# Performance work log

Measured on AMD Instinct MI355X. Metric: run time of the kernel, lower is better.

The kernel has to match this reference:

```python
import jax, jax.numpy as jnp
import numpy as np

B, S, D, E, K = 4, 2048, 1024, 8, 2
H = 4 * D  # FFN hidden per expert


def setup_inputs() -> dict:
    key = jax.random.key(0)
    ks = jax.random.split(key, 5)
    s = 0.02  # init scale
    return {
        "x": jax.random.normal(ks[0], (B, S, D), dtype=jnp.float32),
        "Wg": jax.random.normal(ks[1], (D, E), dtype=jnp.float32) * s,
        "bg": jnp.zeros((E,), dtype=jnp.float32),
        "W1": jax.random.normal(ks[2], (E, D, H), dtype=jnp.float32) * s,
        "b1": jnp.zeros((E, H), dtype=jnp.float32),
        "W2": jax.random.normal(ks[3], (E, H, D), dtype=jnp.float32) * s,
        "b2": jnp.zeros((E, D), dtype=jnp.float32),
    }


def reference(x, Wg, bg, W1, b1, W2, b2):
    # Router: softmax over expert logits, then top-k (torch.topk semantics)
    probs = jax.nn.softmax(x @ Wg + bg, axis=-1)      # [B,S,E]
    w, idx = jax.lax.top_k(probs, K)                   # [B,S,K] each
    # Dense all-experts MLP (matches original: every expert runs on every token)
    h = jax.nn.gelu(jnp.einsum('bsd,edh->bseh', x, W1) + b1, approximate=False)  # [B,S,E,H]
    y = jnp.einsum('bseh,ehd->bsed', h, W2) + b2       # [B,S,E,D]
    # One-hot mask + weighted sum == gather selected experts, scale by w, sum over k
    yk = jnp.take_along_axis(y, idx[..., None], axis=2)  # [B,S,K,D]
    return jnp.sum(yk * w[..., None], axis=2)            # [B,S,D]
```

## Files before the change

### kernel.cpp

```cpp
#include <hip/hip_runtime.h>
#include <hip/hip_bf16.h>
#include <math.h>


#define TOK     8192
#define DMODEL  1024
#define NEXP    8
#define HFF     4096
#define NASSIGN 16384
#define SLOTPAD 16512
#define BM      128
#define BN      128
#define BK      64
#define MAXRT   135

typedef __attribute__((ext_vector_type(8))) short s16x8;
typedef __attribute__((ext_vector_type(4))) float f32x4;

__device__ __forceinline__ void gll16(const void* g, void* l) {
  __builtin_amdgcn_global_load_lds((const __attribute__((address_space(1))) void*)g,
                                   (__attribute__((address_space(3))) void*)l, 16, 0, 0);
}

__global__ void transpose_cvt(const float* __restrict__ in, __hip_bfloat16* __restrict__ out,
                              int R, int C) {
  __shared__ float t[64][65];
  const float* src = in + (size_t)blockIdx.z * R * C;
  __hip_bfloat16* dst = out + (size_t)blockIdx.z * R * C;
  const int r0 = blockIdx.y * 64, c0 = blockIdx.x * 64;
  const int tc = threadIdx.x & 63, tr = threadIdx.x >> 6;
#pragma unroll
  for (int i = 0; i < 16; ++i) {
    int r = i * 4 + tr;
    t[r][tc] = src[(size_t)(r0 + r) * C + c0 + tc];
  }
  __syncthreads();
  const int jl = (threadIdx.x & 15) * 4;
  const int cw = threadIdx.x >> 4;
#pragma unroll
  for (int p = 0; p < 4; ++p) {
    const int cc = p * 16 + cw;
    union { ushort4 u; __hip_bfloat16 h[4]; } o;
#pragma unroll
    for (int u = 0; u < 4; ++u) o.h[u] = __float2bfloat16(t[jl + u][cc]);
    *(ushort4*)(dst + (size_t)(c0 + cc) * R + r0 + jl) = o.u;
  }
}

__global__ void router_kernel(const float* __restrict__ x, const float* __restrict__ Wg,
                              const float* __restrict__ bg, int* __restrict__ idx,
                              float* __restrict__ wtok, int* __restrict__ counts) {
  __shared__ int scnt[NEXP];
  if (threadIdx.x < NEXP) scnt[threadIdx.x] = 0;
  __syncthreads();
  const int wave = threadIdx.x >> 6, lane = threadIdx.x & 63;
  const int t = blockIdx.x * 4 + wave;
  float acc[NEXP];
#pragma unroll
  for (int e = 0; e < NEXP; ++e) acc[e] = 0.f;
  const float* xr = x + (size_t)t * DMODEL + lane * 16;
#pragma unroll
  for (int j = 0; j < 4; ++j) {
    float4 xv = *(const float4*)(xr + j * 4);
    const float* wr = Wg + (size_t)(lane * 16 + j * 4) * NEXP;
#pragma unroll
    for (int u = 0; u < 4; ++u) {
      float xs = (&xv.x)[u];
      float4 w0 = *(const float4*)(wr + u * NEXP);
      float4 w1 = *(const float4*)(wr + u * NEXP + 4);
      acc[0] += xs * w0.x; acc[1] += xs * w0.y; acc[2] += xs * w0.z; acc[3] += xs * w0.w;
      acc[4] += xs * w1.x; acc[5] += xs * w1.y; acc[6] += xs * w1.z; acc[7] += xs * w1.w;
    }
  }
#pragma unroll
  for (int off = 32; off >= 1; off >>= 1) {
#pragma unroll
    for (int e = 0; e < NEXP; ++e) acc[e] += __shfl_xor(acc[e], off, 64);
  }
  if (lane == 0) {
    float l[NEXP], m = -1e30f;
#pragma unroll
    for (int e = 0; e < NEXP; ++e) { l[e] = acc[e] + bg[e]; m = fmaxf(m, l[e]); }
    float p[NEXP], s = 0.f;
#pragma unroll
    for (int e = 0; e < NEXP; ++e) { p[e] = expf(l[e] - m); s += p[e]; }
    float inv = 1.f / s;
#pragma unroll
    for (int e = 0; e < NEXP; ++e) p[e] *= inv;
    int i0 = 0; float v0 = p[0];
#pragma unroll
    for (int e = 1; e < NEXP; ++e) if (p[e] > v0) { v0 = p[e]; i0 = e; }
    int i1 = -1; float v1 = -1e30f;
#pragma unroll
    for (int e = 0; e < NEXP; ++e) if (e != i0 && p[e] > v1) { v1 = p[e]; i1 = e; }
    idx[2 * t] = i0; idx[2 * t + 1] = i1;
    wtok[2 * t] = v0; wtok[2 * t + 1] = v1;
    atomicAdd(&scnt[i0], 1); atomicAdd(&scnt[i1], 1);
  }
  __syncthreads();
  if (threadIdx.x < NEXP) atomicAdd(&counts[threadIdx.x], scnt[threadIdx.x]);
}

__global__ void scan_kernel(int* ctrl) {
  if (threadIdx.x == 0 && blockIdx.x == 0) {
    int* counts = ctrl;
    int* cursor = ctrl + 8;
    int* expOff = ctrl + 16;
    int* tro = ctrl + 26;
    expOff[0] = 0; tro[0] = 0;
    for (int e = 0; e < NEXP; ++e) {
      expOff[e + 1] = expOff[e] + counts[e];
      tro[e + 1] = tro[e] + (counts[e] + BM - 1) / BM;
      cursor[e] = expOff[e];
    }
  }
}

__global__ void scatter_kernel(const int* __restrict__ idx, const float* __restrict__ wtok,
                               int* ctrl, int* __restrict__ perm, float* __restrict__ wslot) {
  __shared__ int lcnt[NEXP];
  __shared__ int lbase[NEXP];
  const int t = blockIdx.x * 256 + threadIdx.x;
  if (threadIdx.x < NEXP) lcnt[threadIdx.x] = 0;
  __syncthreads();
  const int e0 = idx[2 * t], e1 = idx[2 * t + 1];
  const int l0 = atomicAdd(&lcnt[e0], 1);
  const int l1 = atomicAdd(&lcnt[e1], 1);
  __syncthreads();
  if (threadIdx.x < NEXP)
    lbase[threadIdx.x] = atomicAdd(&ctrl[8 + threadIdx.x], lcnt[threadIdx.x]);
  __syncthreads();
  const int s0 = lbase[e0] + l0, s1 = lbase[e1] + l1;
  perm[s0] = t; perm[s1] = t;
  wslot[s0] = wtok[2 * t]; wslot[s1] = wtok[2 * t + 1];
}

__global__ void gather_cvt_x(const float* __restrict__ x, const int* __restrict__ perm,
                             __hip_bfloat16* __restrict__ xg) {
  const int slot = blockIdx.x;
  const int t = perm[slot];
  const float4 v = *(const float4*)(x + (size_t)t * DMODEL + threadIdx.x * 4);
  union { ushort4 u; __hip_bfloat16 h[4]; } o;
  o.h[0] = __float2bfloat16(v.x); o.h[1] = __float2bfloat16(v.y);
  o.h[2] = __float2bfloat16(v.z); o.h[3] = __float2bfloat16(v.w);
  *(ushort4*)(xg + (size_t)slot * DMODEL + threadIdx.x * 4) = o.u;
}


__global__ __launch_bounds__(256, 3) void gemm1_kernel(
    const __hip_bfloat16* __restrict__ xg, const __hip_bfloat16* __restrict__ w1t,
    const float* __restrict__ b1, __hip_bfloat16* __restrict__ hbuf,
    const int* __restrict__ ctrl) {
  const int* expOff = ctrl + 16;
  const int* tro = ctrl + 26;
  const int w = blockIdx.x;
  const int rt = w >> 5, nt = w & 31;
  if (rt >= tro[NEXP]) return;
  int e = 0;
#pragma unroll
  for (int q = 1; q < NEXP; ++q) if (tro[q] <= rt) e = q;
  const int rowBase = expOff[e] + (rt - tro[e]) * BM;
  const int rowEnd = expOff[e + 1];

  __shared__ __hip_bfloat16 lA[BM * BK];
  __shared__ __hip_bfloat16 lB[BN * BK];

  const int tid = threadIdx.x;
  const int lane = tid & 63, wave = tid >> 6;
  const int quad = lane >> 4, lm = lane & 15;
  const int waveM = (wave >> 1) * 64, waveN = (wave & 1) * 64;

  f32x4 acc[4][4];
#pragma unroll
  for (int a = 0; a < 4; ++a)
#pragma unroll
    for (int b = 0; b < 4; ++b) acc[a][b] = (f32x4){0.f, 0.f, 0.f, 0.f};

  const __hip_bfloat16* bbase = w1t + (size_t)e * HFF * DMODEL + (size_t)nt * BN * DMODEL;
  const __hip_bfloat16* gA[4]; const __hip_bfloat16* gB[4];
  __hip_bfloat16* sA[4]; __hip_bfloat16* sB[4];
#pragma unroll
  for (int i = 0; i < 4; ++i) {
    const int s = tid + 256 * i;
    const int r = s >> 3, sl = s & 7, kc = sl ^ (r & 7);
    gA[i] = xg + (size_t)(rowBase + r) * DMODEL + kc * 8;
    gB[i] = bbase + (size_t)r * DMODEL + kc * 8;
    sA[i] = lA + s * 8; sB[i] = lB + s * 8;
  }

  int aOff[4], bOff[4];
#pragma unroll
  for (int tm = 0; tm < 4; ++tm) {
    int r = waveM + tm * 16 + lm;
    aOff[tm] = r * 64 + (quad ^ (r & 7)) * 8;
  }
#pragma unroll
  for (int tn = 0; tn < 4; ++tn) {
    int r = waveN + tn * 16 + lm;
    bOff[tn] = r * 64 + (quad ^ (r & 7)) * 8;
  }

  for (int kt = 0; kt < DMODEL / BK; ++kt) {
#pragma unroll
    for (int i = 0; i < 4; ++i) { gll16(gA[i], sA[i]); gll16(gB[i], sB[i]); }
#pragma unroll
    for (int i = 0; i < 4; ++i) { gA[i] += BK; gB[i] += BK; }
    __syncthreads();
#pragma unroll
    for (int h = 0; h < 2; ++h) {
      s16x8 af[4], bfr[4];
#pragma unroll
      for (int tm = 0; tm < 4; ++tm) af[tm] = *(const s16x8*)(lA + (aOff[tm] ^ (h * 32)));
#pragma unroll
      for (int tn = 0; tn < 4; ++tn) bfr[tn] = *(const s16x8*)(lB + (bOff[tn] ^ (h * 32)));
#pragma unroll
      for (int tm = 0; tm < 4; ++tm)
#pragma unroll
        for (int tn = 0; tn < 4; ++tn)
          acc[tm][tn] = __builtin_amdgcn_mfma_f32_16x16x32_bf16(af[tm], bfr[tn], acc[tm][tn], 0, 0, 0);
    }
    __syncthreads();
  }

  const int colBase = nt * BN + waveN;
  float bv[4];
#pragma unroll
  for (int tn = 0; tn < 4; ++tn) bv[tn] = b1[e * HFF + colBase + tn * 16 + lm];
#pragma unroll
  for (int tm = 0; tm < 4; ++tm) {
    const int rb = rowBase + waveM + tm * 16 + quad * 4;
#pragma unroll
    for (int reg = 0; reg < 4; ++reg) {
      const int row = rb + reg;
      if (row < rowEnd) {
#pragma unroll
        for (int tn = 0; tn < 4; ++tn) {
          float v = acc[tm][tn][reg] + bv[tn];
          v = 0.5f * v * (1.f + erff(v * 0.70710678118654752f));
          hbuf[(size_t)row * HFF + colBase + tn * 16 + lm] = __float2bfloat16(v);
        }
      }
    }
  }
}

__global__ __launch_bounds__(256, 3) void gemm2_kernel(
    const __hip_bfloat16* __restrict__ hbuf, const __hip_bfloat16* __restrict__ w2t,
    const float* __restrict__ b2, const float* __restrict__ wslot,
    const int* __restrict__ perm, float* __restrict__ out, const int* __restrict__ ctrl) {
  const int* expOff = ctrl + 16;
  const int* tro = ctrl + 26;
  const int w = blockIdx.x;
  const int rt = w >> 3, nt = w & 7;
  if (rt >= tro[NEXP]) return;
  int e = 0;
#pragma unroll
  for (int q = 1; q < NEXP; ++q) if (tro[q] <= rt) e = q;
  const int rowBase = expOff[e] + (rt - tro[e]) * BM;
  const int rowEnd = expOff[e + 1];

  __shared__ __hip_bfloat16 lA[BM * BK];
  __shared__ __hip_bfloat16 lB[BN * BK];

  const int tid = threadIdx.x;
  const int lane = tid & 63, wave = tid >> 6;
  const int quad = lane >> 4, lm = lane & 15;
  const int waveM = (wave >> 1) * 64, waveN = (wave & 1) * 64;

  f32x4 acc[4][4];
#pragma unroll
  for (int a = 0; a < 4; ++a)
#pragma unroll
    for (int b = 0; b < 4; ++b) acc[a][b] = (f32x4){0.f, 0.f, 0.f, 0.f};

  const __hip_bfloat16* bbase = w2t + (size_t)e * DMODEL * HFF + (size_t)nt * BN * HFF;
  const __hip_bfloat16* gA[4]; const __hip_bfloat16* gB[4];
  __hip_bfloat16* sA[4]; __hip_bfloat16* sB[4];
#pragma unroll
  for (int i = 0; i < 4; ++i) {
    const int s = tid + 256 * i;
    const int r = s >> 3, sl = s & 7, kc = sl ^ (r & 7);
    gA[i] = hbuf + (size_t)(rowBase + r) * HFF + kc * 8;
    gB[i] = bbase + (size_t)r * HFF + kc * 8;
    sA[i] = lA + s * 8; sB[i] = lB + s * 8;
  }

  int aOff[4], bOff[4];
#pragma unroll
  for (int tm = 0; tm < 4; ++tm) {
    int r = waveM + tm * 16 + lm;
    aOff[tm] = r * 64 + (quad ^ (r & 7)) * 8;
  }
#pragma unroll
  for (int tn = 0; tn < 4; ++tn) {
    int r = waveN + tn * 16 + lm;
    bOff[tn] = r * 64 + (quad ^ (r & 7)) * 8;
  }

  for (int kt = 0; kt < HFF / BK; ++kt) {
#pragma unroll
    for (int i = 0; i < 4; ++i) { gll16(gA[i], sA[i]); gll16(gB[i], sB[i]); }
#pragma unroll
    for (int i = 0; i < 4; ++i) { gA[i] += BK; gB[i] += BK; }
    __syncthreads();
#pragma unroll
    for (int h = 0; h < 2; ++h) {
      s16x8 af[4], bfr[4];
#pragma unroll
      for (int tm = 0; tm < 4; ++tm) af[tm] = *(const s16x8*)(lA + (aOff[tm] ^ (h * 32)));
#pragma unroll
      for (int tn = 0; tn < 4; ++tn) bfr[tn] = *(const s16x8*)(lB + (bOff[tn] ^ (h * 32)));
#pragma unroll
      for (int tm = 0; tm < 4; ++tm)
#pragma unroll
        for (int tn = 0; tn < 4; ++tn)
          acc[tm][tn] = __builtin_amdgcn_mfma_f32_16x16x32_bf16(af[tm], bfr[tn], acc[tm][tn], 0, 0, 0);
    }
    __syncthreads();
  }

  const int colBase = nt * BN + waveN;
  float bv[4];
#pragma unroll
  for (int tn = 0; tn < 4; ++tn) bv[tn] = b2[e * DMODEL + colBase + tn * 16 + lm];
#pragma unroll
  for (int tm = 0; tm < 4; ++tm) {
    const int rb = rowBase + waveM + tm * 16 + quad * 4;
#pragma unroll
    for (int reg = 0; reg < 4; ++reg) {
      const int row = rb + reg;
      if (row < rowEnd) {
        const float wr = wslot[row];
        float* orow = out + (size_t)perm[row] * DMODEL + colBase;
#pragma unroll
        for (int tn = 0; tn < 4; ++tn)
          atomicAdd(orow + tn * 16 + lm, (acc[tm][tn][reg] + bv[tn]) * wr);
      }
    }
  }
}

extern "C" void kernel_launch(void* const* d_in, const int* in_sizes, int n_in,
                              void* d_out, int out_size, void* d_ws, size_t ws_size,
                              hipStream_t stream) {
  const float* x  = (const float*)d_in[0];
  const float* Wg = (const float*)d_in[1];
  const float* bg = (const float*)d_in[2];
  const float* W1 = (const float*)d_in[3];
  const float* b1 = (const float*)d_in[4];
  const float* W2 = (const float*)d_in[5];
  const float* b2 = (const float*)d_in[6];
  float* out = (float*)d_out;

  char* ws = (char*)d_ws;
  size_t off = 0;
  auto take = [&](size_t bytes) -> char* {
    char* p = ws + off;
    off = (off + bytes + 255) & ~(size_t)255;
    return p;
  };
  int*   ctrl  = (int*)take(64 * sizeof(int));
  int*   idx   = (int*)take((size_t)TOK * 2 * 4);
  float* wtok  = (float*)take((size_t)TOK * 2 * 4);
  int*   perm  = (int*)take((size_t)SLOTPAD * 4);
  float* wslot = (float*)take((size_t)SLOTPAD * 4);
  __hip_bfloat16* W1t = (__hip_bfloat16*)take((size_t)NEXP * HFF * DMODEL * 2);
  __hip_bfloat16* W2t = (__hip_bfloat16*)take((size_t)NEXP * DMODEL * HFF * 2);
  __hip_bfloat16* xgb = (__hip_bfloat16*)take((size_t)SLOTPAD * DMODEL * 2);
  __hip_bfloat16* hb  = (__hip_bfloat16*)take((size_t)SLOTPAD * HFF * 2);
  (void)ws_size; (void)in_sizes; (void)n_in; (void)out_size;

  hipMemsetAsync(ctrl, 0, 64 * sizeof(int), stream);
  hipMemsetAsync(out, 0, (size_t)TOK * DMODEL * 4, stream);
  transpose_cvt<<<dim3(HFF / 64, DMODEL / 64, NEXP), 256, 0, stream>>>(W1, W1t, DMODEL, HFF);
  transpose_cvt<<<dim3(DMODEL / 64, HFF / 64, NEXP), 256, 0, stream>>>(W2, W2t, HFF, DMODEL);
  router_kernel<<<TOK / 4, 256, 0, stream>>>(x, Wg, bg, idx, wtok, ctrl);
  scan_kernel<<<1, 64, 0, stream>>>(ctrl);
  scatter_kernel<<<TOK / 256, 256, 0, stream>>>(idx, wtok, ctrl, perm, wslot);
  gather_cvt_x<<<NASSIGN, 256, 0, stream>>>(x, perm, xgb);
  gemm1_kernel<<<MAXRT * (HFF / BN), 256, 0, stream>>>(xgb, W1t, b1, hb, ctrl);
  gemm2_kernel<<<MAXRT * (DMODEL / BN), 256, 0, stream>>>(hb, W2t, b2, wslot, perm, out, ctrl);
}
```

Baseline: 793.5 us.

## Use 256x256 tiles with double-buffered LDS pipeline and split-K in gemm2

```diff
diff --git a/kernel.cpp b/kernel.cpp
--- a/kernel.cpp
+++ b/kernel.cpp
@@ -8,11 +8,11 @@
 #define NEXP    8
 #define HFF     4096
 #define NASSIGN 16384
-#define SLOTPAD 16512
-#define BM      128
-#define BN      128
+#define SLOTPAD 16640
+#define BM      256
+#define BN      256
 #define BK      64
-#define MAXRT   135
+#define MAXRT   71
 
 typedef __attribute__((ext_vector_type(8))) short s16x8;
 typedef __attribute__((ext_vector_type(4))) float f32x4;
@@ -21,6 +21,18 @@
   __builtin_amdgcn_global_load_lds((const __attribute__((address_space(1))) void*)g,
                                    (__attribute__((address_space(3))) void*)l, 16, 0, 0);
 }
+
+#define MFMA_Q(AFR, BFR, ACC)                                                   \
+  do {                                                                          \
+    __builtin_amdgcn_s_setprio(1);                                              \
+    _Pragma("unroll") for (int tm_ = 0; tm_ < 4; ++tm_) {                       \
+      _Pragma("unroll") for (int tn_ = 0; tn_ < 4; ++tn_) {                     \
+        (ACC)[tm_][tn_] = __builtin_amdgcn_mfma_f32_16x16x32_bf16(              \
+            (AFR)[tm_], (BFR)[tn_], (ACC)[tm_][tn_], 0, 0, 0);                  \
+      }                                                                         \
+    }                                                                           \
+    __builtin_amdgcn_s_setprio(0);                                              \
+  } while (0)
 
 __global__ void transpose_cvt(const float* __restrict__ in, __hip_bfloat16* __restrict__ out,
                               int R, int C) {
@@ -147,14 +159,14 @@
 }
 
 
-__global__ __launch_bounds__(256, 3) void gemm1_kernel(
+__global__ __launch_bounds__(512, 2) void gemm1_kernel(
     const __hip_bfloat16* __restrict__ xg, const __hip_bfloat16* __restrict__ w1t,
     const float* __restrict__ b1, __hip_bfloat16* __restrict__ hbuf,
     const int* __restrict__ ctrl) {
   const int* expOff = ctrl + 16;
   const int* tro = ctrl + 26;
   const int w = blockIdx.x;
-  const int rt = w >> 5, nt = w & 31;
+  const int rt = w >> 4, nt = w & 15;
   if (rt >= tro[NEXP]) return;
   int e = 0;
 #pragma unroll
@@ -162,73 +174,102 @@
   const int rowBase = expOff[e] + (rt - tro[e]) * BM;
   const int rowEnd = expOff[e + 1];
 
-  __shared__ __hip_bfloat16 lA[BM * BK];
-  __shared__ __hip_bfloat16 lB[BN * BK];
+  __shared__ __hip_bfloat16 lA[2 * 16384];
+  __shared__ __hip_bfloat16 lB[2 * 16384];
 
   const int tid = threadIdx.x;
   const int lane = tid & 63, wave = tid >> 6;
   const int quad = lane >> 4, lm = lane & 15;
-  const int waveM = (wave >> 1) * 64, waveN = (wave & 1) * 64;
-
-  f32x4 acc[4][4];
-#pragma unroll
-  for (int a = 0; a < 4; ++a)
+  const int wm = wave >> 2, wn = wave & 3;
+  const int sw = (quad ^ (lm & 7)) * 8;
+  const int aOff0 = wm * 8192 + lm * 64 + sw;
+  const int bOff0 = (wn >> 1) * 8192 + ((wn & 1) * 64 + lm) * 64 + sw;
+
+  f32x4 acc[8][4];
+#pragma unroll
+  for (int a = 0; a < 8; ++a)
 #pragma unroll
     for (int b = 0; b < 4; ++b) acc[a][b] = (f32x4){0.f, 0.f, 0.f, 0.f};
 
   const __hip_bfloat16* bbase = w1t + (size_t)e * HFF * DMODEL + (size_t)nt * BN * DMODEL;
-  const __hip_bfloat16* gA[4]; const __hip_bfloat16* gB[4];
-  __hip_bfloat16* sA[4]; __hip_bfloat16* sB[4];
-#pragma unroll
-  for (int i = 0; i < 4; ++i) {
-    const int s = tid + 256 * i;
-    const int r = s >> 3, sl = s & 7, kc = sl ^ (r & 7);
-    gA[i] = xg + (size_t)(rowBase + r) * DMODEL + kc * 8;
-    gB[i] = bbase + (size_t)r * DMODEL + kc * 8;
-    sA[i] = lA + s * 8; sB[i] = lB + s * 8;
-  }
-
-  int aOff[4], bOff[4];
-#pragma unroll
-  for (int tm = 0; tm < 4; ++tm) {
-    int r = waveM + tm * 16 + lm;
-    aOff[tm] = r * 64 + (quad ^ (r & 7)) * 8;
-  }
-#pragma unroll
-  for (int tn = 0; tn < 4; ++tn) {
-    int r = waveN + tn * 16 + lm;
-    bOff[tn] = r * 64 + (quad ^ (r & 7)) * 8;
-  }
-
-  for (int kt = 0; kt < DMODEL / BK; ++kt) {
-#pragma unroll
-    for (int i = 0; i < 4; ++i) { gll16(gA[i], sA[i]); gll16(gB[i], sB[i]); }
-#pragma unroll
-    for (int i = 0; i < 4; ++i) { gA[i] += BK; gB[i] += BK; }
-    __syncthreads();
-#pragma unroll
-    for (int h = 0; h < 2; ++h) {
-      s16x8 af[4], bfr[4];
-#pragma unroll
-      for (int tm = 0; tm < 4; ++tm) af[tm] = *(const s16x8*)(lA + (aOff[tm] ^ (h * 32)));
-#pragma unroll
-      for (int tn = 0; tn < 4; ++tn) bfr[tn] = *(const s16x8*)(lB + (bOff[tn] ^ (h * 32)));
-#pragma unroll
-      for (int tm = 0; tm < 4; ++tm)
-#pragma unroll
-        for (int tn = 0; tn < 4; ++tn)
-          acc[tm][tn] = __builtin_amdgcn_mfma_f32_16x16x32_bf16(af[tm], bfr[tn], acc[tm][tn], 0, 0, 0);
-    }
-    __syncthreads();
-  }
-
-  const int colBase = nt * BN + waveN;
+  const __hip_bfloat16* gA0;
+  const __hip_bfloat16* gB0;
+  {
+    const int r = tid >> 3, kc = (tid & 7) ^ (r & 7);
+    gA0 = xg + (size_t)(rowBase + r) * DMODEL + kc * 8;
+    gB0 = bbase + (size_t)r * DMODEL + kc * 8;
+  }
+  const int dBase = tid * 8;
+
+  auto stageA = [&](int buf) {
+#pragma unroll
+    for (int j = 0; j < 4; ++j)
+      gll16(gA0 + (size_t)j * 64 * DMODEL, lA + buf * 16384 + dBase + j * 4096);
+    gA0 += BK;
+  };
+  auto stageB = [&](int buf) {
+#pragma unroll
+    for (int j = 0; j < 4; ++j)
+      gll16(gB0 + (size_t)j * 64 * DMODEL, lB + buf * 16384 + dBase + j * 4096);
+    gB0 += BK;
+  };
+
+  stageA(0); stageB(0); stageA(1); stageB(1);
+  asm volatile("s_waitcnt vmcnt(8)" ::: "memory");
+  __builtin_amdgcn_s_barrier();
+
+  const int NT = DMODEL / BK;
+  for (int t = 0; t < NT; ++t) {
+    const int c = t & 1;
+    const int cb = c * 16384;
+    s16x8 aA[8], bA[4], aB[8], bB[4];
+    {
+      const __hip_bfloat16* pa = lA + cb + aOff0;
+      const __hip_bfloat16* pb = lB + cb + bOff0;
+#pragma unroll
+      for (int tm = 0; tm < 8; ++tm) aA[tm] = *(const s16x8*)(pa + tm * 1024);
+#pragma unroll
+      for (int tn = 0; tn < 4; ++tn) bA[tn] = *(const s16x8*)(pb + tn * 1024);
+    }
+    __builtin_amdgcn_s_barrier();
+    asm volatile("s_waitcnt lgkmcnt(0)" ::: "memory");
+    MFMA_Q(aA, bA, acc);
+    __builtin_amdgcn_s_barrier();
+    {
+      const __hip_bfloat16* pa = lA + cb + (aOff0 ^ 32);
+      const __hip_bfloat16* pb = lB + cb + (bOff0 ^ 32);
+#pragma unroll
+      for (int tm = 0; tm < 8; ++tm) aB[tm] = *(const s16x8*)(pa + tm * 1024);
+#pragma unroll
+      for (int tn = 0; tn < 4; ++tn) bB[tn] = *(const s16x8*)(pb + tn * 1024);
+    }
+    __builtin_amdgcn_s_barrier();
+    asm volatile("s_waitcnt lgkmcnt(0)" ::: "memory");
+    MFMA_Q((aA + 4), bA, (acc + 4));
+    __builtin_amdgcn_s_barrier();
+    asm volatile("" ::: "memory");
+    if (t + 2 < NT) stageA(c);
+    __builtin_amdgcn_s_barrier();
+    MFMA_Q(aB, bB, acc);
+    __builtin_amdgcn_s_barrier();
+    if (t + 2 < NT) stageB(c);
+    __builtin_amdgcn_s_barrier();
+    MFMA_Q((aB + 4), bB, (acc + 4));
+    __builtin_amdgcn_s_barrier();
+    if (t < NT - 1) {
+      if (t + 2 < NT) asm volatile("s_waitcnt vmcnt(8)" ::: "memory");
+      else            asm volatile("s_waitcnt vmcnt(0)" ::: "memory");
+      __builtin_amdgcn_s_barrier();
+    }
+  }
+
+  const int colBase = nt * BN + wn * 64;
   float bv[4];
 #pragma unroll
   for (int tn = 0; tn < 4; ++tn) bv[tn] = b1[e * HFF + colBase + tn * 16 + lm];
 #pragma unroll
-  for (int tm = 0; tm < 4; ++tm) {
-    const int rb = rowBase + waveM + tm * 16 + quad * 4;
+  for (int tm = 0; tm < 8; ++tm) {
+    const int rb = rowBase + wm * 128 + tm * 16 + quad * 4;
 #pragma unroll
     for (int reg = 0; reg < 4; ++reg) {
       const int row = rb + reg;
@@ -244,14 +285,16 @@
   }
 }
 
-__global__ __launch_bounds__(256, 3) void gemm2_kernel(
+__global__ __launch_bounds__(512, 2) void gemm2_kernel(
     const __hip_bfloat16* __restrict__ hbuf, const __hip_bfloat16* __restrict__ w2t,
     const float* __restrict__ b2, const float* __restrict__ wslot,
     const int* __restrict__ perm, float* __restrict__ out, const int* __restrict__ ctrl) {
   const int* expOff = ctrl + 16;
   const int* tro = ctrl + 26;
   const int w = blockIdx.x;
-  const int rt = w >> 3, nt = w & 7;
+  const int ks = w & 1;
+  const int nt = (w >> 1) & 3;
+  const int rt = w >> 3;
   if (rt >= tro[NEXP]) return;
   int e = 0;
 #pragma unroll
@@ -259,73 +302,104 @@
   const int rowBase = expOff[e] + (rt - tro[e]) * BM;
   const int rowEnd = expOff[e + 1];
 
-  __shared__ __hip_bfloat16 lA[BM * BK];
-  __shared__ __hip_bfloat16 lB[BN * BK];
+  __shared__ __hip_bfloat16 lA[2 * 16384];
+  __shared__ __hip_bfloat16 lB[2 * 16384];
 
   const int tid = threadIdx.x;
   const int lane = tid & 63, wave = tid >> 6;
   const int quad = lane >> 4, lm = lane & 15;
-  const int waveM = (wave >> 1) * 64, waveN = (wave & 1) * 64;
-
-  f32x4 acc[4][4];
-#pragma unroll
-  for (int a = 0; a < 4; ++a)
+  const int wm = wave >> 2, wn = wave & 3;
+  const int sw = (quad ^ (lm & 7)) * 8;
+  const int aOff0 = wm * 8192 + lm * 64 + sw;
+  const int bOff0 = (wn >> 1) * 8192 + ((wn & 1) * 64 + lm) * 64 + sw;
+
+  f32x4 acc[8][4];
+#pragma unroll
+  for (int a = 0; a < 8; ++a)
 #pragma unroll
     for (int b = 0; b < 4; ++b) acc[a][b] = (f32x4){0.f, 0.f, 0.f, 0.f};
 
+  const int NT = (HFF / BK) / 2;
+  const int kBase = ks * NT * BK;
   const __hip_bfloat16* bbase = w2t + (size_t)e * DMODEL * HFF + (size_t)nt * BN * HFF;
-  const __hip_bfloat16* gA[4]; const __hip_bfloat16* gB[4];
-  __hip_bfloat16* sA[4]; __hip_bfloat16* sB[4];
-#pragma unroll
-  for (int i = 0; i < 4; ++i) {
-    const int s = tid + 256 * i;
-    const int r = s >> 3, sl = s & 7, kc = sl ^ (r & 7);
-    gA[i] = hbuf + (size_t)(rowBase + r) * HFF + kc * 8;
-    gB[i] = bbase + (size_t)r * HFF + kc * 8;
-    sA[i] = lA + s * 8; sB[i] = lB + s * 8;
-  }
-
-  int aOff[4], bOff[4];
-#pragma unroll
-  for (int tm = 0; tm < 4; ++tm) {
-    int r = waveM + tm * 16 + lm;
-    aOff[tm] = r * 64 + (quad ^ (r & 7)) * 8;
-  }
-#pragma unroll
-  for (int tn = 0; tn < 4; ++tn) {
-    int r = waveN + tn * 16 + lm;
-    bOff[tn] = r * 64 + (quad ^ (r & 7)) * 8;
-  }
-
-  for (int kt = 0; kt < HFF / BK; ++kt) {
-#pragma unroll
-    for (int i = 0; i < 4; ++i) { gll16(gA[i], sA[i]); gll16(gB[i], sB[i]); }
-#pragma unroll
-    for (int i = 0; i < 4; ++i) { gA[i] += BK; gB[i] += BK; }
-    __syncthreads();
-#pragma unroll
-    for (int h = 0; h < 2; ++h) {
-      s16x8 af[4], bfr[4];
-#pragma unroll
-      for (int tm = 0; tm < 4; ++tm) af[tm] = *(const s16x8*)(lA + (aOff[tm] ^ (h * 32)));
-#pragma unroll
-      for (int tn = 0; tn < 4; ++tn) bfr[tn] = *(const s16x8*)(lB + (bOff[tn] ^ (h * 32)));
-#pragma unroll
-      for (int tm = 0; tm < 4; ++tm)
-#pragma unroll
-        for (int tn = 0; tn < 4; ++tn)
-          acc[tm][tn] = __builtin_amdgcn_mfma_f32_16x16x32_bf16(af[tm], bfr[tn], acc[tm][tn], 0, 0, 0);
-    }
-    __syncthreads();
-  }
-
-  const int colBase = nt * BN + waveN;
+  const __hip_bfloat16* gA0;
+  const __hip_bfloat16* gB0;
+  {
+    const int r = tid >> 3, kc = (tid & 7) ^ (r & 7);
+    gA0 = hbuf + (size_t)(rowBase + r) * HFF + kBase + kc * 8;
+    gB0 = bbase + (size_t)r * HFF + kBase + kc * 8;
+  }
+  const int dBase = tid * 8;
+
+  auto stageA = [&](int buf) {
+#pragma unroll
+    for (int j = 0; j < 4; ++j)
+      gll16(gA0 + (size_t)j * 64 * HFF, lA + buf * 16384 + dBase + j * 4096);
+    gA0 += BK;
+  };
+  auto stageB = [&](int buf) {
+#pragma unroll
+    for (int j = 0; j < 4; ++j)
+      gll16(gB0 + (size_t)j * 64 * HFF, lB + buf * 16384 + dBase + j * 4096);
+    gB0 += BK;
+  };
+
+  stageA(0); stageB(0); stageA(1); stageB(1);
+  asm volatile("s_waitcnt vmcnt(8)" ::: "memory");
+  __builtin_amdgcn_s_barrier();
+
+  for (int t = 0; t < NT; ++t) {
+    const int c = t & 1;
+    const int cb = c * 16384;
+    s16x8 aA[8], bA[4], aB[8], bB[4];
+    {
+      const __hip_bfloat16* pa = lA + cb + aOff0;
+      const __hip_bfloat16* pb = lB + cb + bOff0;
+#pragma unroll
+      for (int tm = 0; tm < 8; ++tm) aA[tm] = *(const s16x8*)(pa + tm * 1024);
+#pragma unroll
+      for (int tn = 0; tn < 4; ++tn) bA[tn] = *(const s16x8*)(pb + tn * 1024);
+    }
+    __builtin_amdgcn_s_barrier();
+    asm volatile("s_waitcnt lgkmcnt(0)" ::: "memory");
+    MFMA_Q(aA, bA, acc);
+    __builtin_amdgcn_s_barrier();
+    {
+      const __hip_bfloat16* pa = lA + cb + (aOff0 ^ 32);
+      const __hip_bfloat16* pb = lB + cb + (bOff0 ^ 32);
+#pragma unroll
+      for (int tm = 0; tm < 8; ++tm) aB[tm] = *(const s16x8*)(pa + tm * 1024);
+#pragma unroll
+      for (int tn = 0; tn < 4; ++tn) bB[tn] = *(const s16x8*)(pb + tn * 1024);
+    }
+    __builtin_amdgcn_s_barrier();
+    asm volatile("s_waitcnt lgkmcnt(0)" ::: "memory");
+    MFMA_Q((aA + 4), bA, (acc + 4));
+    __builtin_amdgcn_s_barrier();
+    asm volatile("" ::: "memory");
+    if (t + 2 < NT) stageA(c);
+    __builtin_amdgcn_s_barrier();
+    MFMA_Q(aB, bB, acc);
+    __builtin_amdgcn_s_barrier();
+    if (t + 2 < NT) stageB(c);
+    __builtin_amdgcn_s_barrier();
+    MFMA_Q((aB + 4), bB, (acc + 4));
+    __builtin_amdgcn_s_barrier();
+    if (t < NT - 1) {
+      if (t + 2 < NT) asm volatile("s_waitcnt vmcnt(8)" ::: "memory");
+      else            asm volatile("s_waitcnt vmcnt(0)" ::: "memory");
+      __builtin_amdgcn_s_barrier();
+    }
+  }
+
+  const int colBase = nt * BN + wn * 64;
   float bv[4];
 #pragma unroll
-  for (int tn = 0; tn < 4; ++tn) bv[tn] = b2[e * DMODEL + colBase + tn * 16 + lm];
-#pragma unroll
-  for (int tm = 0; tm < 4; ++tm) {
-    const int rb = rowBase + waveM + tm * 16 + quad * 4;
+  for (int tn = 0; tn < 4; ++tn)
+    bv[tn] = ks ? 0.f : b2[e * DMODEL + colBase + tn * 16 + lm];
+#pragma unroll
+  for (int tm = 0; tm < 8; ++tm) {
+    const int rb = rowBase + wm * 128 + tm * 16 + quad * 4;
 #pragma unroll
     for (int reg = 0; reg < 4; ++reg) {
       const int row = rb + reg;
@@ -378,6 +452,6 @@
   scan_kernel<<<1, 64, 0, stream>>>(ctrl);
   scatter_kernel<<<TOK / 256, 256, 0, stream>>>(idx, wtok, ctrl, perm, wslot);
   gather_cvt_x<<<NASSIGN, 256, 0, stream>>>(x, perm, xgb);
-  gemm1_kernel<<<MAXRT * (HFF / BN), 256, 0, stream>>>(xgb, W1t, b1, hb, ctrl);
-  gemm2_kernel<<<MAXRT * (DMODEL / BN), 256, 0, stream>>>(hb, W2t, b2, wslot, perm, out, ctrl);
-}
+  gemm1_kernel<<<MAXRT * (HFF / BN), 512, 0, stream>>>(xgb, W1t, b1, hb, ctrl);
+  gemm2_kernel<<<MAXRT * (DMODEL / BN) * 2, 512, 0, stream>>>(hb, W2t, b2, wslot, perm, out, ctrl);
+}
```

New measurement: 929.2 us. +17.1%, slower.

## Use 256x256 double-buffered pipelined GEMM tiles with split-K for second GEMM

Applied to the files above, without the earlier changes.

```diff
diff --git a/kernel.cpp b/kernel.cpp
--- a/kernel.cpp
+++ b/kernel.cpp
@@ -8,11 +8,11 @@
 #define NEXP    8
 #define HFF     4096
 #define NASSIGN 16384
-#define SLOTPAD 16512
-#define BM      128
-#define BN      128
+#define SLOTPAD 16640
+#define BM      256
+#define BN      256
 #define BK      64
-#define MAXRT   135
+#define MAXRT   71
 
 typedef __attribute__((ext_vector_type(8))) short s16x8;
 typedef __attribute__((ext_vector_type(4))) float f32x4;
@@ -21,6 +21,45 @@
   __builtin_amdgcn_global_load_lds((const __attribute__((address_space(1))) void*)g,
                                    (__attribute__((address_space(3))) void*)l, 16, 0, 0);
 }
+
+#define BAR   __builtin_amdgcn_s_barrier()
+#define LGKM0 do { asm volatile("s_waitcnt lgkmcnt(0)" ::: "memory"); \
+                   __builtin_amdgcn_sched_barrier(0); } while (0)
+#define VMW4  asm volatile("s_waitcnt vmcnt(4)" ::: "memory")
+#define VMW0  asm volatile("s_waitcnt vmcnt(0)" ::: "memory")
+
+#define READ_A(H)                                                       \
+  { const __hip_bfloat16* pa_ = lAc + (H) * 8192;                       \
+    _Pragma("unroll") for (int tm = 0; tm < 4; ++tm) {                  \
+      aF0[tm] = *(const s16x8*)(pa_ + aoff[tm]);                        \
+      aF1[tm] = *(const s16x8*)(pa_ + (aoff[tm] ^ 32)); } }
+
+#define READ_B(H)                                                       \
+  { const __hip_bfloat16* pb_ = lBc + (H) * 8192;                       \
+    _Pragma("unroll") for (int tn = 0; tn < 2; ++tn) {                  \
+      bF0[tn] = *(const s16x8*)(pb_ + boff[tn]);                        \
+      bF1[tn] = *(const s16x8*)(pb_ + (boff[tn] ^ 32)); } }
+
+#define STAGE_A(H)                                                      \
+  { const __hip_bfloat16* s_ = gA + (size_t)(H) * 128 * LDA + kN;       \
+    __hip_bfloat16* d_ = lAn + (H) * 8192 + dBase;                      \
+    gll16(s_, d_); gll16(s_ + (size_t)64 * LDA, d_ + 4096); }
+
+#define STAGE_B(H)                                                      \
+  { const __hip_bfloat16* s_ = gB + (size_t)(H) * 128 * LDB + kN;       \
+    __hip_bfloat16* d_ = lBn + (H) * 8192 + dBase;                      \
+    gll16(s_, d_); gll16(s_ + (size_t)64 * LDB, d_ + 4096); }
+
+#define MFMA_PH(Q)                                                      \
+  __builtin_amdgcn_s_setprio(1);                                        \
+  _Pragma("unroll") for (int tm = 0; tm < 4; ++tm)                      \
+    _Pragma("unroll") for (int tn = 0; tn < 2; ++tn) {                  \
+      acc[Q][tm][tn] = __builtin_amdgcn_mfma_f32_16x16x32_bf16(         \
+          aF0[tm], bF0[tn], acc[Q][tm][tn], 0, 0, 0);                   \
+      acc[Q][tm][tn] = __builtin_amdgcn_mfma_f32_16x16x32_bf16(         \
+          aF1[tm], bF1[tn], acc[Q][tm][tn], 0, 0, 0);                   \
+    }                                                                   \
+  __builtin_amdgcn_s_setprio(0);
 
 __global__ void transpose_cvt(const float* __restrict__ in, __hip_bfloat16* __restrict__ out,
                               int R, int C) {
@@ -147,14 +186,14 @@
 }
 
 
-__global__ __launch_bounds__(256, 3) void gemm1_kernel(
+__global__ __launch_bounds__(512, 2) void gemm1_kernel(
     const __hip_bfloat16* __restrict__ xg, const __hip_bfloat16* __restrict__ w1t,
     const float* __restrict__ b1, __hip_bfloat16* __restrict__ hbuf,
     const int* __restrict__ ctrl) {
   const int* expOff = ctrl + 16;
   const int* tro = ctrl + 26;
   const int w = blockIdx.x;
-  const int rt = w >> 5, nt = w & 31;
+  const int rt = w >> 4, nt = w & 15;
   if (rt >= tro[NEXP]) return;
   int e = 0;
 #pragma unroll
@@ -162,96 +201,113 @@
   const int rowBase = expOff[e] + (rt - tro[e]) * BM;
   const int rowEnd = expOff[e + 1];
 
-  __shared__ __hip_bfloat16 lA[BM * BK];
-  __shared__ __hip_bfloat16 lB[BN * BK];
+  __shared__ __hip_bfloat16 lA[2 * 16384];
+  __shared__ __hip_bfloat16 lB[2 * 16384];
 
   const int tid = threadIdx.x;
   const int lane = tid & 63, wave = tid >> 6;
   const int quad = lane >> 4, lm = lane & 15;
-  const int waveM = (wave >> 1) * 64, waveN = (wave & 1) * 64;
-
-  f32x4 acc[4][4];
+  const int wm2 = wave >> 2, wn2 = wave & 3;
+  const int dBase = tid * 8;
+
+  int aoff[4], boff[2];
+#pragma unroll
+  for (int tm = 0; tm < 4; ++tm) {
+    int r = wm2 * 64 + tm * 16 + lm;
+    aoff[tm] = r * 64 + ((quad ^ (r & 7)) << 3);
+  }
+#pragma unroll
+  for (int tn = 0; tn < 2; ++tn) {
+    int r = wn2 * 32 + tn * 16 + lm;
+    boff[tn] = r * 64 + ((quad ^ (r & 7)) << 3);
+  }
+
+  f32x4 acc[4][4][2];
 #pragma unroll
   for (int a = 0; a < 4; ++a)
 #pragma unroll
-    for (int b = 0; b < 4; ++b) acc[a][b] = (f32x4){0.f, 0.f, 0.f, 0.f};
-
-  const __hip_bfloat16* bbase = w1t + (size_t)e * HFF * DMODEL + (size_t)nt * BN * DMODEL;
-  const __hip_bfloat16* gA[4]; const __hip_bfloat16* gB[4];
-  __hip_bfloat16* sA[4]; __hip_bfloat16* sB[4];
-#pragma unroll
-  for (int i = 0; i < 4; ++i) {
-    const int s = tid + 256 * i;
-    const int r = s >> 3, sl = s & 7, kc = sl ^ (r & 7);
-    gA[i] = xg + (size_t)(rowBase + r) * DMODEL + kc * 8;
-    gB[i] = bbase + (size_t)r * DMODEL + kc * 8;
-    sA[i] = lA + s * 8; sB[i] = lB + s * 8;
-  }
-
-  int aOff[4], bOff[4];
-#pragma unroll
-  for (int tm = 0; tm < 4; ++tm) {
-    int r = waveM + tm * 16 + lm;
-    aOff[tm] = r * 64 + (quad ^ (r & 7)) * 8;
-  }
-#pragma unroll
-  for (int tn = 0; tn < 4; ++tn) {
-    int r = waveN + tn * 16 + lm;
-    bOff[tn] = r * 64 + (quad ^ (r & 7)) * 8;
-  }
-
-  for (int kt = 0; kt < DMODEL / BK; ++kt) {
-#pragma unroll
-    for (int i = 0; i < 4; ++i) { gll16(gA[i], sA[i]); gll16(gB[i], sB[i]); }
-#pragma unroll
-    for (int i = 0; i < 4; ++i) { gA[i] += BK; gB[i] += BK; }
-    __syncthreads();
-#pragma unroll
-    for (int h = 0; h < 2; ++h) {
-      s16x8 af[4], bfr[4];
-#pragma unroll
-      for (int tm = 0; tm < 4; ++tm) af[tm] = *(const s16x8*)(lA + (aOff[tm] ^ (h * 32)));
-#pragma unroll
-      for (int tn = 0; tn < 4; ++tn) bfr[tn] = *(const s16x8*)(lB + (bOff[tn] ^ (h * 32)));
-#pragma unroll
-      for (int tm = 0; tm < 4; ++tm)
-#pragma unroll
-        for (int tn = 0; tn < 4; ++tn)
-          acc[tm][tn] = __builtin_amdgcn_mfma_f32_16x16x32_bf16(af[tm], bfr[tn], acc[tm][tn], 0, 0, 0);
-    }
-    __syncthreads();
-  }
-
-  const int colBase = nt * BN + waveN;
-  float bv[4];
-#pragma unroll
-  for (int tn = 0; tn < 4; ++tn) bv[tn] = b1[e * HFF + colBase + tn * 16 + lm];
-#pragma unroll
-  for (int tm = 0; tm < 4; ++tm) {
-    const int rb = rowBase + waveM + tm * 16 + quad * 4;
-#pragma unroll
-    for (int reg = 0; reg < 4; ++reg) {
-      const int row = rb + reg;
-      if (row < rowEnd) {
-#pragma unroll
-        for (int tn = 0; tn < 4; ++tn) {
-          float v = acc[tm][tn][reg] + bv[tn];
-          v = 0.5f * v * (1.f + erff(v * 0.70710678118654752f));
-          hbuf[(size_t)row * HFF + colBase + tn * 16 + lm] = __float2bfloat16(v);
+    for (int b = 0; b < 4; ++b)
+#pragma unroll
+      for (int c = 0; c < 2; ++c) acc[a][b][c] = (f32x4){0.f, 0.f, 0.f, 0.f};
+
+  const int LDA = DMODEL, LDB = DMODEL;
+  const __hip_bfloat16* gA;
+  const __hip_bfloat16* gB;
+  {
+    const int rS = tid >> 3, kcS = (tid & 7) ^ ((tid >> 3) & 7);
+    gA = xg + (size_t)(rowBase + rS) * LDA + kcS * 8;
+    gB = w1t + (size_t)e * HFF * DMODEL + (size_t)nt * BN * LDB
+             + (size_t)rS * LDB + kcS * 8;
+  }
+
+  {
+    __hip_bfloat16* lAn = lA; __hip_bfloat16* lBn = lB;
+    const int kN = 0;
+    STAGE_A(0); STAGE_B(0); STAGE_A(1); STAGE_B(1);
+    VMW0; BAR;
+  }
+
+  const int NT = DMODEL / BK;
+  for (int t = 0; t < NT; ++t) {
+    const __hip_bfloat16* lAc = lA + (t & 1) * 16384;
+    const __hip_bfloat16* lBc = lB + (t & 1) * 16384;
+    __hip_bfloat16* lAn = lA + ((t + 1) & 1) * 16384;
+    __hip_bfloat16* lBn = lB + ((t + 1) & 1) * 16384;
+    const int kN = (t + 1) * BK;
+    const bool pf = (t + 1 < NT);
+    s16x8 aF0[4], aF1[4], bF0[2], bF1[2];
+    READ_A(0); READ_B(0); if (pf) STAGE_A(0);
+    BAR; LGKM0; MFMA_PH(0); VMW4; BAR;
+    READ_B(1); if (pf) STAGE_B(0);
+    BAR; LGKM0; MFMA_PH(1); VMW4; BAR;
+    READ_A(1); if (pf) STAGE_B(1);
+    BAR; LGKM0; MFMA_PH(2); VMW4; BAR;
+    READ_B(0); if (pf) STAGE_A(1);
+    BAR; LGKM0; MFMA_PH(3);
+    if (t + 2 < NT) { VMW4; } else { VMW0; }
+    BAR;
+  }
+
+  const int colB = nt * BN;
+  float bvv[2][2];
+#pragma unroll
+  for (int qn = 0; qn < 2; ++qn)
+#pragma unroll
+    for (int tn = 0; tn < 2; ++tn)
+      bvv[qn][tn] = b1[e * HFF + colB + qn * 128 + wn2 * 32 + tn * 16 + lm];
+#pragma unroll
+  for (int qi = 0; qi < 4; ++qi) {
+    const int QM = qi >> 1, QN = (qi & 1) ^ (qi >> 1);
+#pragma unroll
+    for (int tm = 0; tm < 4; ++tm) {
+      const int rb = rowBase + QM * 128 + wm2 * 64 + tm * 16 + quad * 4;
+#pragma unroll
+      for (int reg = 0; reg < 4; ++reg) {
+        const int row = rb + reg;
+        if (row < rowEnd) {
+#pragma unroll
+          for (int tn = 0; tn < 2; ++tn) {
+            float v = acc[qi][tm][tn][reg] + bvv[QN][tn];
+            v = 0.5f * v * (1.f + erff(v * 0.70710678118654752f));
+            hbuf[(size_t)row * HFF + colB + QN * 128 + wn2 * 32 + tn * 16 + lm] =
+                __float2bfloat16(v);
+          }
         }
       }
     }
   }
 }
 
-__global__ __launch_bounds__(256, 3) void gemm2_kernel(
+__global__ __launch_bounds__(512, 2) void gemm2_kernel(
     const __hip_bfloat16* __restrict__ hbuf, const __hip_bfloat16* __restrict__ w2t,
     const float* __restrict__ b2, const float* __restrict__ wslot,
     const int* __restrict__ perm, float* __restrict__ out, const int* __restrict__ ctrl) {
   const int* expOff = ctrl + 16;
   const int* tro = ctrl + 26;
   const int w = blockIdx.x;
-  const int rt = w >> 3, nt = w & 7;
+  const int ks = w & 1;
+  const int nt = (w >> 1) & 3;
+  const int rt = w >> 3;
   if (rt >= tro[NEXP]) return;
   int e = 0;
 #pragma unroll
@@ -259,82 +315,98 @@
   const int rowBase = expOff[e] + (rt - tro[e]) * BM;
   const int rowEnd = expOff[e + 1];
 
-  __shared__ __hip_bfloat16 lA[BM * BK];
-  __shared__ __hip_bfloat16 lB[BN * BK];
+  __shared__ __hip_bfloat16 lA[2 * 16384];
+  __shared__ __hip_bfloat16 lB[2 * 16384];
 
   const int tid = threadIdx.x;
   const int lane = tid & 63, wave = tid >> 6;
   const int quad = lane >> 4, lm = lane & 15;
-  const int waveM = (wave >> 1) * 64, waveN = (wave & 1) * 64;
-
-  f32x4 acc[4][4];
+  const int wm2 = wave >> 2, wn2 = wave & 3;
+  const int dBase = tid * 8;
+
+  int aoff[4], boff[2];
+#pragma unroll
+  for (int tm = 0; tm < 4; ++tm) {
+    int r = wm2 * 64 + tm * 16 + lm;
+    aoff[tm] = r * 64 + ((quad ^ (r & 7)) << 3);
+  }
+#pragma unroll
+  for (int tn = 0; tn < 2; ++tn) {
+    int r = wn2 * 32 + tn * 16 + lm;
+    boff[tn] = r * 64 + ((quad ^ (r & 7)) << 3);
+  }
+
+  f32x4 acc[4][4][2];
 #pragma unroll
   for (int a = 0; a < 4; ++a)
 #pragma unroll
-    for (int b = 0; b < 4; ++b) acc[a][b] = (f32x4){0.f, 0.f, 0.f, 0.f};
-
-  const __hip_bfloat16* bbase = w2t + (size_t)e * DMODEL * HFF + (size_t)nt * BN * HFF;
-  const __hip_bfloat16* gA[4]; const __hip_bfloat16* gB[4];
-  __hip_bfloat16* sA[4]; __hip_bfloat16* sB[4];
-#pragma unroll
-  for (int i = 0; i < 4; ++i) {
-    const int s = tid + 256 * i;
-    const int r = s >> 3, sl = s & 7, kc = sl ^ (r & 7);
-    gA[i] = hbuf + (size_t)(rowBase + r) * HFF + kc * 8;
-    gB[i] = bbase + (size_t)r * HFF + kc * 8;
-    sA[i] = lA + s * 8; sB[i] = lB + s * 8;
-  }
-
-  int aOff[4], bOff[4];
-#pragma unroll
-  for (int tm = 0; tm < 4; ++tm) {
-    int r = waveM + tm * 16 + lm;
-    aOff[tm] = r * 64 + (quad ^ (r & 7)) * 8;
-  }
-#pragma unroll
-  for (int tn = 0; tn < 4; ++tn) {
-    int r = waveN + tn * 16 + lm;
-    bOff[tn] = r * 64 + (quad ^ (r & 7)) * 8;
-  }
-
-  for (int kt = 0; kt < HFF / BK; ++kt) {
-#pragma unroll
-    for (int i = 0; i < 4; ++i) { gll16(gA[i], sA[i]); gll16(gB[i], sB[i]); }
-#pragma unroll
-    for (int i = 0; i < 4; ++i) { gA[i] += BK; gB[i] += BK; }
-    __syncthreads();
-#pragma unroll
-    for (int h = 0; h < 2; ++h) {
-      s16x8 af[4], bfr[4];
-#pragma unroll
-      for (int tm = 0; tm < 4; ++tm) af[tm] = *(const s16x8*)(lA + (aOff[tm] ^ (h * 32)));
-#pragma unroll
-      for (int tn = 0; tn < 4; ++tn) bfr[tn] = *(const s16x8*)(lB + (bOff[tn] ^ (h * 32)));
-#pragma unroll
-      for (int tm = 0; tm < 4; ++tm)
-#pragma unroll
-        for (int tn = 0; tn < 4; ++tn)
-          acc[tm][tn] = __builtin_amdgcn_mfma_f32_16x16x32_bf16(af[tm], bfr[tn], acc[tm][tn], 0, 0, 0);
-    }
-    __syncthreads();
-  }
-
-  const int colBase = nt * BN + waveN;
-  float bv[4];
-#pragma unroll
-  for (int tn = 0; tn < 4; ++tn) bv[tn] = b2[e * DMODEL + colBase + tn * 16 + lm];
-#pragma unroll
-  for (int tm = 0; tm < 4; ++tm) {
-    const int rb = rowBase + waveM + tm * 16 + quad * 4;
-#pragma unroll
-    for (int reg = 0; reg < 4; ++reg) {
-      const int row = rb + reg;
-      if (row < rowEnd) {
-        const float wr = wslot[row];
-        float* orow = out + (size_t)perm[row] * DMODEL + colBase;
-#pragma unroll
-        for (int tn = 0; tn < 4; ++tn)
-          atomicAdd(orow + tn * 16 + lm, (acc[tm][tn][reg] + bv[tn]) * wr);
+    for (int b = 0; b < 4; ++b)
+#pragma unroll
+      for (int c = 0; c < 2; ++c) acc[a][b][c] = (f32x4){0.f, 0.f, 0.f, 0.f};
+
+  const int NT = (HFF / BK) / 2;
+  const int kBase = ks * NT * BK;
+  const int LDA = HFF, LDB = HFF;
+  const __hip_bfloat16* gA;
+  const __hip_bfloat16* gB;
+  {
+    const int rS = tid >> 3, kcS = (tid & 7) ^ ((tid >> 3) & 7);
+    gA = hbuf + (size_t)(rowBase + rS) * LDA + kBase + kcS * 8;
+    gB = w2t + (size_t)e * DMODEL * HFF + (size_t)nt * BN * LDB
+             + (size_t)rS * LDB + kBase + kcS * 8;
+  }
+
+  {
+    __hip_bfloat16* lAn = lA; __hip_bfloat16* lBn = lB;
+    const int kN = 0;
+    STAGE_A(0); STAGE_B(0); STAGE_A(1); STAGE_B(1);
+    VMW0; BAR;
+  }
+
+  for (int t = 0; t < NT; ++t) {
+    const __hip_bfloat16* lAc = lA + (t & 1) * 16384;
+    const __hip_bfloat16* lBc = lB + (t & 1) * 16384;
+    __hip_bfloat16* lAn = lA + ((t + 1) & 1) * 16384;
+    __hip_bfloat16* lBn = lB + ((t + 1) & 1) * 16384;
+    const int kN = (t + 1) * BK;
+    const bool pf = (t + 1 < NT);
+    s16x8 aF0[4], aF1[4], bF0[2], bF1[2];
+    READ_A(0); READ_B(0); if (pf) STAGE_A(0);
+    BAR; LGKM0; MFMA_PH(0); VMW4; BAR;
+    READ_B(1); if (pf) STAGE_B(0);
+    BAR; LGKM0; MFMA_PH(1); VMW4; BAR;
+    READ_A(1); if (pf) STAGE_B(1);
+    BAR; LGKM0; MFMA_PH(2); VMW4; BAR;
+    READ_B(0); if (pf) STAGE_A(1);
+    BAR; LGKM0; MFMA_PH(3);
+    if (t + 2 < NT) { VMW4; } else { VMW0; }
+    BAR;
+  }
+
+  const int colB = nt * BN;
+  float bvv[2][2];
+#pragma unroll
+  for (int qn = 0; qn < 2; ++qn)
+#pragma unroll
+    for (int tn = 0; tn < 2; ++tn)
+      bvv[qn][tn] = ks ? 0.f : b2[e * DMODEL + colB + qn * 128 + wn2 * 32 + tn * 16 + lm];
+#pragma unroll
+  for (int qi = 0; qi < 4; ++qi) {
+    const int QM = qi >> 1, QN = (qi & 1) ^ (qi >> 1);
+#pragma unroll
+    for (int tm = 0; tm < 4; ++tm) {
+      const int rb = rowBase + QM * 128 + wm2 * 64 + tm * 16 + quad * 4;
+#pragma unroll
+      for (int reg = 0; reg < 4; ++reg) {
+        const int row = rb + reg;
+        if (row < rowEnd) {
+          const float wr = wslot[row];
+          float* orow = out + (size_t)perm[row] * DMODEL + colB;
+#pragma unroll
+          for (int tn = 0; tn < 2; ++tn)
+            atomicAdd(orow + QN * 128 + wn2 * 32 + tn * 16 + lm,
+                      (acc[qi][tm][tn][reg] + bvv[QN][tn]) * wr);
+        }
       }
     }
   }
@@ -378,6 +450,6 @@
   scan_kernel<<<1, 64, 0, stream>>>(ctrl);
   scatter_kernel<<<TOK / 256, 256, 0, stream>>>(idx, wtok, ctrl, perm, wslot);
   gather_cvt_x<<<NASSIGN, 256, 0, stream>>>(x, perm, xgb);
-  gemm1_kernel<<<MAXRT * (HFF / BN), 256, 0, stream>>>(xgb, W1t, b1, hb, ctrl);
-  gemm2_kernel<<<MAXRT * (DMODEL / BN), 256, 0, stream>>>(hb, W2t, b2, wslot, perm, out, ctrl);
-}
+  gemm1_kernel<<<MAXRT * (HFF / BN), 512, 0, stream>>>(xgb, W1t, b1, hb, ctrl);
+  gemm2_kernel<<<MAXRT * (DMODEL / BN) * 2, 512, 0, stream>>>(hb, W2t, b2, wslot, perm, out, ctrl);
+}
```

After: 938.9 us. +18.3%, slower.
